# Performance work log

Hardware: AMD Instinct MI355X
Metric: run time of the kernel (lower is better)

Reference implementation:

```python
import jax, jax.numpy as jnp
import numpy as np

B, Q, K, QS, KS, H, DV = 16, 128, 512, 256, 256, 128, 256


def setup_inputs() -> dict:
    key = jax.random.key(0)
    ks = jax.random.split(key, 7)
    return {
        "queries": jax.random.normal(ks[0], (B, Q, QS), dtype=jnp.float32),
        "keys": jax.random.normal(ks[1], (B, K, KS), dtype=jnp.float32),
        "values": jax.random.normal(ks[2], (B, K, DV), dtype=jnp.float32),
        "valid_lens": jax.random.randint(ks[3], (B,), 1, K + 1),
        # Linear weights (no bias); stored as [in, hidden] so x @ W == nn.Linear
        "W_q": jax.random.normal(ks[4], (QS, H), dtype=jnp.float32) / np.float32(np.sqrt(QS)),
        "W_k": jax.random.normal(ks[5], (KS, H), dtype=jnp.float32) / np.float32(np.sqrt(KS)),
        "w_v": jax.random.normal(ks[6], (H,), dtype=jnp.float32) / np.float32(np.sqrt(H)),
    }


def reference(queries, keys, values, valid_lens, W_q, W_k, w_v):
    # Projections
    q = jnp.einsum('bqd,dh->bqh', queries, W_q)   # [B,Q,H]
    k = jnp.einsum('bkd,dh->bkh', keys, W_k)      # [B,K,H]
    # Additive (Bahdanau) score: tanh(q + k) . w_v  -> [B,Q,K]
    feats = jnp.tanh(q[:, :, None, :] + k[:, None, :, :])  # [B,Q,K,H] big intermediate
    scores = jnp.einsum('bqkh,h->bqk', feats, w_v)
    # masked softmax over keys: positions >= valid_len get -1e6 (as in torch ref)
    mask = jnp.arange(K)[None, None, :] < valid_lens[:, None, None]  # [B,1,K] bcast
    scores = jnp.where(mask, scores, jnp.float32(-1e6))
    attn = jax.nn.softmax(scores, axis=-1)        # [B,Q,K]
    # dropout p=0.0 -> identity
    return jnp.einsum('bqk,bkd->bqd', attn, values)  # [B,Q,DV]
```

## Files before the change

### kernel.cpp

```cpp
#include <hip/hip_runtime.h>
#include <hip/hip_bf16.h>

#define NB 16
#define NQ 128
#define NK 512
#define DIN 256
#define NH 128
#define NDV 256

#define CSC 2.8853900817779268f

__global__ __launch_bounds__(256) void proj_both_kernel(
    const float* __restrict__ Q, const float* __restrict__ K,
    const float* __restrict__ Wq, const float* __restrict__ Wk,
    float* __restrict__ QP, float* __restrict__ KPT)
{
    __shared__ float Xl[32 * DIN];
    const int tid = threadIdx.x;
    int blk = blockIdx.x;
    const float* X; const float* W;
    int b, r0, isq;
    if (blk < 64) { isq = 1; b = blk >> 2; r0 = (blk & 3) * 32;
                    X = Q + ((size_t)b * NQ + r0) * DIN; W = Wq; }
    else { blk -= 64; isq = 0; b = blk >> 4; r0 = (blk & 15) * 32;
           X = K + ((size_t)b * NK + r0) * DIN; W = Wk; }

    {
        const float4* Xg = (const float4*)X;
        float4* Xs = (float4*)Xl;
        #pragma unroll
        for (int i = 0; i < 8; ++i) Xs[tid + 256 * i] = Xg[tid + 256 * i];
    }
    __syncthreads();

    const int h4 = tid & 31;
    const int rg = tid >> 5;
    const float4* Wv = (const float4*)W;

    float4 acc[4];
    #pragma unroll
    for (int r = 0; r < 4; ++r) { acc[r].x = 0.f; acc[r].y = 0.f; acc[r].z = 0.f; acc[r].w = 0.f; }

    float4 w0 = Wv[0 * 32 + h4], w1 = Wv[1 * 32 + h4], w2 = Wv[2 * 32 + h4], w3 = Wv[3 * 32 + h4];
    float4 n0 = Wv[4 * 32 + h4], n1 = Wv[5 * 32 + h4], n2 = Wv[6 * 32 + h4], n3 = Wv[7 * 32 + h4];
    for (int d = 0; d < DIN; d += 4) {
        const int dp = (d + 8 < DIN) ? d + 8 : 0;
        float4 m0 = Wv[(dp + 0) * 32 + h4];
        float4 m1 = Wv[(dp + 1) * 32 + h4];
        float4 m2 = Wv[(dp + 2) * 32 + h4];
        float4 m3 = Wv[(dp + 3) * 32 + h4];
        #pragma unroll
        for (int r = 0; r < 4; ++r) {
            float4 x = *(const float4*)&Xl[(rg * 4 + r) * DIN + d];
            acc[r].x += x.x * w0.x + x.y * w1.x + x.z * w2.x + x.w * w3.x;
            acc[r].y += x.x * w0.y + x.y * w1.y + x.z * w2.y + x.w * w3.y;
            acc[r].z += x.x * w0.z + x.y * w1.z + x.z * w2.z + x.w * w3.z;
            acc[r].w += x.x * w0.w + x.y * w1.w + x.z * w2.w + x.w * w3.w;
        }
        w0 = n0; w1 = n1; w2 = n2; w3 = n3;
        n0 = m0; n1 = m1; n2 = m2; n3 = m3;
    }
    #pragma unroll
    for (int r = 0; r < 4; ++r) {
        acc[r].x *= CSC; acc[r].y *= CSC; acc[r].z *= CSC; acc[r].w *= CSC;
    }

    if (isq) {
        #pragma unroll
        for (int r = 0; r < 4; ++r)
            *(float4*)&QP[((size_t)b * NQ + r0 + rg * 4 + r) * NH + 4 * h4] = acc[r];
    } else {
        float* T = Xl;
        __syncthreads();
        #pragma unroll
        for (int r = 0; r < 4; ++r) {
            T[(4 * h4 + 0) * 36 + rg * 4 + r] = acc[r].x;
            T[(4 * h4 + 1) * 36 + rg * 4 + r] = acc[r].y;
            T[(4 * h4 + 2) * 36 + rg * 4 + r] = acc[r].z;
            T[(4 * h4 + 3) * 36 + rg * 4 + r] = acc[r].w;
        }
        __syncthreads();
        #pragma unroll
        for (int i = 0; i < 4; ++i) {
            const int idx = tid + 256 * i;
            const int h = idx >> 3, c8 = idx & 7;
            float4 v = *(const float4*)&T[h * 36 + c8 * 4];
            *(float4*)&KPT[((size_t)b * NH + h) * NK + r0 + c8 * 4] = v;
        }
    }
}

__global__ __launch_bounds__(512) void attn_fused_kernel(
    const float* __restrict__ QP, const float* __restrict__ KPT,
    const float* __restrict__ wv, const int* __restrict__ vlen,
    const float* __restrict__ V, float* __restrict__ OUT)
{
    __shared__ float qcl[4 * NH];
    __shared__ float wvl[NH];
    __shared__ float sc[4][NK];
    __shared__ float part[4][4][NDV];
    const int tid = threadIdx.x;
    const int b  = blockIdx.x & 15;
    const int q0 = (blockIdx.x >> 4) * 4;

    qcl[tid] = QP[((size_t)b * NQ + q0) * NH + tid];
    if (tid < NH) wvl[tid] = -2.0f * wv[tid];
    __syncthreads();

    int vl = vlen[b];
    vl = vl < 1 ? 1 : (vl > NK ? NK : vl);

    {
        const float* kb = KPT + (size_t)b * NH * NK + tid;
        float a0 = 0.f, a1 = 0.f, a2 = 0.f, a3 = 0.f;
        #pragma unroll 4
        for (int h = 0; h < NH; ++h) {
            float kv = kb[(size_t)h * NK];
            float wq = wvl[h];
            float e0 = __builtin_amdgcn_exp2f(qcl[0 * NH + h] + kv);
            float e1 = __builtin_amdgcn_exp2f(qcl[1 * NH + h] + kv);
            float e2 = __builtin_amdgcn_exp2f(qcl[2 * NH + h] + kv);
            float e3 = __builtin_amdgcn_exp2f(qcl[3 * NH + h] + kv);
            a0 += wq * __builtin_amdgcn_rcpf(e0 + 1.0f);
            a1 += wq * __builtin_amdgcn_rcpf(e1 + 1.0f);
            a2 += wq * __builtin_amdgcn_rcpf(e2 + 1.0f);
            a3 += wq * __builtin_amdgcn_rcpf(e3 + 1.0f);
        }
        const bool vld = (tid < vl);
        sc[0][tid] = vld ? a0 : -1e6f;
        sc[1][tid] = vld ? a1 : -1e6f;
        sc[2][tid] = vld ? a2 : -1e6f;
        sc[3][tid] = vld ? a3 : -1e6f;
    }
    __syncthreads();

    const int w = tid >> 6, lane = tid & 63;
    if (w < 4) {
        float vals[8];
        float m = -3.0e38f;
        #pragma unroll
        for (int i = 0; i < 8; ++i) { vals[i] = sc[w][lane + 64 * i]; m = fmaxf(m, vals[i]); }
        #pragma unroll
        for (int off = 32; off; off >>= 1) m = fmaxf(m, __shfl_xor(m, off, 64));
        float s = 0.f;
        #pragma unroll
        for (int i = 0; i < 8; ++i) {
            vals[i] = __builtin_amdgcn_exp2f((vals[i] - m) * 1.4426950408889634f);
            s += vals[i];
        }
        #pragma unroll
        for (int off = 32; off; off >>= 1) s += __shfl_xor(s, off, 64);
        const float invs = 1.0f / s;
        #pragma unroll
        for (int i = 0; i < 8; ++i) sc[w][lane + 64 * i] = vals[i] * invs;
    }
    __syncthreads();

    float4 o[4];
    #pragma unroll
    for (int r = 0; r < 4; ++r) { o[r].x = 0.f; o[r].y = 0.f; o[r].z = 0.f; o[r].w = 0.f; }
    {
        const float* vb = V + (size_t)b * NK * NDV + lane * 4;
        const int kb0 = w * 64;
        #pragma unroll 4
        for (int kk = 0; kk < 64; ++kk) {
            const int k = kb0 + kk;
            float4 v4 = *(const float4*)(vb + (size_t)k * NDV);
            float p0 = sc[0][k], p1 = sc[1][k], p2 = sc[2][k], p3 = sc[3][k];
            o[0].x += p0 * v4.x; o[0].y += p0 * v4.y; o[0].z += p0 * v4.z; o[0].w += p0 * v4.w;
            o[1].x += p1 * v4.x; o[1].y += p1 * v4.y; o[1].z += p1 * v4.z; o[1].w += p1 * v4.w;
            o[2].x += p2 * v4.x; o[2].y += p2 * v4.y; o[2].z += p2 * v4.z; o[2].w += p2 * v4.w;
            o[3].x += p3 * v4.x; o[3].y += p3 * v4.y; o[3].z += p3 * v4.z; o[3].w += p3 * v4.w;
        }
    }
    if (w >= 4) {
        #pragma unroll
        for (int r = 0; r < 4; ++r) *(float4*)&part[w - 4][r][lane * 4] = o[r];
    }
    __syncthreads();
    if (w < 4) {
        #pragma unroll
        for (int r = 0; r < 4; ++r) {
            float4 t = *(const float4*)&part[w][r][lane * 4];
            o[r].x += t.x; o[r].y += t.y; o[r].z += t.z; o[r].w += t.w;
            *(float4*)&part[w][r][lane * 4] = o[r];
        }
    }
    __syncthreads();
    if (tid < 256) {
        const int r = tid >> 6, d4 = tid & 63;
        float4 s = {0.f, 0.f, 0.f, 0.f};
        #pragma unroll
        for (int p = 0; p < 4; ++p) {
            float4 q = *(const float4*)&part[p][r][d4 * 4];
            s.x += q.x; s.y += q.y; s.z += q.z; s.w += q.w;
        }
        *(float4*)&OUT[((size_t)b * NQ + q0 + r) * NDV + d4 * 4] = s;
    }
}

extern "C" void kernel_launch(void* const* d_in, const int* in_sizes, int n_in,
                              void* d_out, int out_size, void* d_ws, size_t ws_size,
                              hipStream_t stream) {
    const float* queries = (const float*)d_in[0];
    const float* keys    = (const float*)d_in[1];
    const float* values  = (const float*)d_in[2];
    const int*   vlen    = (const int*)d_in[3];
    const float* Wq      = (const float*)d_in[4];
    const float* Wk      = (const float*)d_in[5];
    const float* wv      = (const float*)d_in[6];
    float* out           = (float*)d_out;

    float* qp  = (float*)d_ws;
    float* kpt = qp + (size_t)NB * NQ * NH;

    proj_both_kernel<<<64 + 256, 256, 0, stream>>>(queries, keys, Wq, Wk, qp, kpt);
    attn_fused_kernel<<<NB * 32, 512, 0, stream>>>(qp, kpt, wv, vlen, values, out);
}
```

Measured before the change: 131.6 us.

## Skip softmax max pass, defer normalization, prefetch keys, halve projection tiles

The attention kernel now exponentiates raw scores directly, with no max subtraction. This relies on the score being bounded, since it is a w_v-weighted sum of tanh values. Normalization by the row sum is deferred to the final output write, which removes one shared-memory pass and a reduction. The score loop gets explicit register prefetching of the next four key-projection rows. The projection kernel processes 16 rows per block instead of 32, doubling the grid for better CU occupancy. The trade-off is possible overflow if w_v has very large magnitude.

After: 135.1 us. 2.7% more time.

```diff
diff --git a/kernel.cpp b/kernel.cpp
--- a/kernel.cpp
+++ b/kernel.cpp
@@ -9,27 +9,28 @@
 #define NDV 256
 
 #define CSC 2.8853900817779268f
+#define L2E 1.4426950408889634f
 
 __global__ __launch_bounds__(256) void proj_both_kernel(
     const float* __restrict__ Q, const float* __restrict__ K,
     const float* __restrict__ Wq, const float* __restrict__ Wk,
     float* __restrict__ QP, float* __restrict__ KPT)
 {
-    __shared__ float Xl[32 * DIN];
+    __shared__ float Xl[16 * DIN];
     const int tid = threadIdx.x;
     int blk = blockIdx.x;
     const float* X; const float* W;
     int b, r0, isq;
-    if (blk < 64) { isq = 1; b = blk >> 2; r0 = (blk & 3) * 32;
-                    X = Q + ((size_t)b * NQ + r0) * DIN; W = Wq; }
-    else { blk -= 64; isq = 0; b = blk >> 4; r0 = (blk & 15) * 32;
+    if (blk < 128) { isq = 1; b = blk >> 3; r0 = (blk & 7) * 16;
+                     X = Q + ((size_t)b * NQ + r0) * DIN; W = Wq; }
+    else { blk -= 128; isq = 0; b = blk >> 5; r0 = (blk & 31) * 16;
            X = K + ((size_t)b * NK + r0) * DIN; W = Wk; }
 
     {
         const float4* Xg = (const float4*)X;
         float4* Xs = (float4*)Xl;
         #pragma unroll
-        for (int i = 0; i < 8; ++i) Xs[tid + 256 * i] = Xg[tid + 256 * i];
+        for (int i = 0; i < 4; ++i) Xs[tid + 256 * i] = Xg[tid + 256 * i];
     }
     __syncthreads();
 
@@ -37,9 +38,9 @@
     const int rg = tid >> 5;
     const float4* Wv = (const float4*)W;
 
-    float4 acc[4];
+    float4 acc[2];
     #pragma unroll
-    for (int r = 0; r < 4; ++r) { acc[r].x = 0.f; acc[r].y = 0.f; acc[r].z = 0.f; acc[r].w = 0.f; }
+    for (int r = 0; r < 2; ++r) { acc[r].x = 0.f; acc[r].y = 0.f; acc[r].z = 0.f; acc[r].w = 0.f; }
 
     float4 w0 = Wv[0 * 32 + h4], w1 = Wv[1 * 32 + h4], w2 = Wv[2 * 32 + h4], w3 = Wv[3 * 32 + h4];
     float4 n0 = Wv[4 * 32 + h4], n1 = Wv[5 * 32 + h4], n2 = Wv[6 * 32 + h4], n3 = Wv[7 * 32 + h4];
@@ -50,8 +51,8 @@
         float4 m2 = Wv[(dp + 2) * 32 + h4];
         float4 m3 = Wv[(dp + 3) * 32 + h4];
         #pragma unroll
-        for (int r = 0; r < 4; ++r) {
-            float4 x = *(const float4*)&Xl[(rg * 4 + r) * DIN + d];
+        for (int r = 0; r < 2; ++r) {
+            float4 x = *(const float4*)&Xl[(rg * 2 + r) * DIN + d];
             acc[r].x += x.x * w0.x + x.y * w1.x + x.z * w2.x + x.w * w3.x;
             acc[r].y += x.x * w0.y + x.y * w1.y + x.z * w2.y + x.w * w3.y;
             acc[r].z += x.x * w0.z + x.y * w1.z + x.z * w2.z + x.w * w3.z;
@@ -61,31 +62,31 @@
         n0 = m0; n1 = m1; n2 = m2; n3 = m3;
     }
     #pragma unroll
-    for (int r = 0; r < 4; ++r) {
+    for (int r = 0; r < 2; ++r) {
         acc[r].x *= CSC; acc[r].y *= CSC; acc[r].z *= CSC; acc[r].w *= CSC;
     }
 
     if (isq) {
         #pragma unroll
-        for (int r = 0; r < 4; ++r)
-            *(float4*)&QP[((size_t)b * NQ + r0 + rg * 4 + r) * NH + 4 * h4] = acc[r];
+        for (int r = 0; r < 2; ++r)
+            *(float4*)&QP[((size_t)b * NQ + r0 + rg * 2 + r) * NH + 4 * h4] = acc[r];
     } else {
         float* T = Xl;
         __syncthreads();
         #pragma unroll
-        for (int r = 0; r < 4; ++r) {
-            T[(4 * h4 + 0) * 36 + rg * 4 + r] = acc[r].x;
-            T[(4 * h4 + 1) * 36 + rg * 4 + r] = acc[r].y;
-            T[(4 * h4 + 2) * 36 + rg * 4 + r] = acc[r].z;
-            T[(4 * h4 + 3) * 36 + rg * 4 + r] = acc[r].w;
+        for (int r = 0; r < 2; ++r) {
+            T[(4 * h4 + 0) * 20 + rg * 2 + r] = acc[r].x;
+            T[(4 * h4 + 1) * 20 + rg * 2 + r] = acc[r].y;
+            T[(4 * h4 + 2) * 20 + rg * 2 + r] = acc[r].z;
+            T[(4 * h4 + 3) * 20 + rg * 2 + r] = acc[r].w;
         }
         __syncthreads();
         #pragma unroll
-        for (int i = 0; i < 4; ++i) {
+        for (int i = 0; i < 2; ++i) {
             const int idx = tid + 256 * i;
-            const int h = idx >> 3, c8 = idx & 7;
-            float4 v = *(const float4*)&T[h * 36 + c8 * 4];
-            *(float4*)&KPT[((size_t)b * NH + h) * NK + r0 + c8 * 4] = v;
+            const int h = idx >> 2, c4 = idx & 3;
+            float4 v = *(const float4*)&T[h * 20 + c4 * 4];
+            *(float4*)&KPT[((size_t)b * NH + h) * NK + r0 + c4 * 4] = v;
         }
     }
 }
@@ -99,6 +100,7 @@
     __shared__ float wvl[NH];
     __shared__ float sc[4][NK];
     __shared__ float part[4][4][NDV];
+    __shared__ float sinv[4];
     const int tid = threadIdx.x;
     const int b  = blockIdx.x & 15;
     const int q0 = (blockIdx.x >> 4) * 4;
@@ -113,46 +115,44 @@
     {
         const float* kb = KPT + (size_t)b * NH * NK + tid;
         float a0 = 0.f, a1 = 0.f, a2 = 0.f, a3 = 0.f;
-        #pragma unroll 4
-        for (int h = 0; h < NH; ++h) {
-            float kv = kb[(size_t)h * NK];
-            float wq = wvl[h];
-            float e0 = __builtin_amdgcn_exp2f(qcl[0 * NH + h] + kv);
-            float e1 = __builtin_amdgcn_exp2f(qcl[1 * NH + h] + kv);
-            float e2 = __builtin_amdgcn_exp2f(qcl[2 * NH + h] + kv);
-            float e3 = __builtin_amdgcn_exp2f(qcl[3 * NH + h] + kv);
-            a0 += wq * __builtin_amdgcn_rcpf(e0 + 1.0f);
-            a1 += wq * __builtin_amdgcn_rcpf(e1 + 1.0f);
-            a2 += wq * __builtin_amdgcn_rcpf(e2 + 1.0f);
-            a3 += wq * __builtin_amdgcn_rcpf(e3 + 1.0f);
+        float c0 = kb[0 * NK], c1 = kb[1 * NK], c2 = kb[2 * NK], c3 = kb[3 * NK];
+        for (int h = 0; h < NH; h += 4) {
+            const int hp = (h + 4 < NH) ? h + 4 : 0;
+            float p0 = kb[(size_t)(hp + 0) * NK];
+            float p1 = kb[(size_t)(hp + 1) * NK];
+            float p2 = kb[(size_t)(hp + 2) * NK];
+            float p3 = kb[(size_t)(hp + 3) * NK];
+            #pragma unroll
+            for (int j = 0; j < 4; ++j) {
+                const float kv = (j == 0) ? c0 : (j == 1) ? c1 : (j == 2) ? c2 : c3;
+                const float wq = wvl[h + j];
+                float e0 = __builtin_amdgcn_exp2f(qcl[0 * NH + h + j] + kv);
+                float e1 = __builtin_amdgcn_exp2f(qcl[1 * NH + h + j] + kv);
+                float e2 = __builtin_amdgcn_exp2f(qcl[2 * NH + h + j] + kv);
+                float e3 = __builtin_amdgcn_exp2f(qcl[3 * NH + h + j] + kv);
+                a0 += wq * __builtin_amdgcn_rcpf(e0 + 1.0f);
+                a1 += wq * __builtin_amdgcn_rcpf(e1 + 1.0f);
+                a2 += wq * __builtin_amdgcn_rcpf(e2 + 1.0f);
+                a3 += wq * __builtin_amdgcn_rcpf(e3 + 1.0f);
+            }
+            c0 = p0; c1 = p1; c2 = p2; c3 = p3;
         }
         const bool vld = (tid < vl);
-        sc[0][tid] = vld ? a0 : -1e6f;
-        sc[1][tid] = vld ? a1 : -1e6f;
-        sc[2][tid] = vld ? a2 : -1e6f;
-        sc[3][tid] = vld ? a3 : -1e6f;
+        sc[0][tid] = vld ? __builtin_amdgcn_exp2f(a0 * L2E) : 0.f;
+        sc[1][tid] = vld ? __builtin_amdgcn_exp2f(a1 * L2E) : 0.f;
+        sc[2][tid] = vld ? __builtin_amdgcn_exp2f(a2 * L2E) : 0.f;
+        sc[3][tid] = vld ? __builtin_amdgcn_exp2f(a3 * L2E) : 0.f;
     }
     __syncthreads();
 
     const int w = tid >> 6, lane = tid & 63;
     if (w < 4) {
-        float vals[8];
-        float m = -3.0e38f;
-        #pragma unroll
-        for (int i = 0; i < 8; ++i) { vals[i] = sc[w][lane + 64 * i]; m = fmaxf(m, vals[i]); }
-        #pragma unroll
-        for (int off = 32; off; off >>= 1) m = fmaxf(m, __shfl_xor(m, off, 64));
         float s = 0.f;
         #pragma unroll
-        for (int i = 0; i < 8; ++i) {
-            vals[i] = __builtin_amdgcn_exp2f((vals[i] - m) * 1.4426950408889634f);
-            s += vals[i];
-        }
+        for (int i = 0; i < 8; ++i) s += sc[w][lane + 64 * i];
         #pragma unroll
         for (int off = 32; off; off >>= 1) s += __shfl_xor(s, off, 64);
-        const float invs = 1.0f / s;
-        #pragma unroll
-        for (int i = 0; i < 8; ++i) sc[w][lane + 64 * i] = vals[i] * invs;
+        if (lane == 0) sinv[w] = __builtin_amdgcn_rcpf(s);
     }
     __syncthreads();
 
@@ -189,12 +189,14 @@
     __syncthreads();
     if (tid < 256) {
         const int r = tid >> 6, d4 = tid & 63;
+        const float iv = sinv[r];
         float4 s = {0.f, 0.f, 0.f, 0.f};
         #pragma unroll
         for (int p = 0; p < 4; ++p) {
             float4 q = *(const float4*)&part[p][r][d4 * 4];
             s.x += q.x; s.y += q.y; s.z += q.z; s.w += q.w;
         }
+        s.x *= iv; s.y *= iv; s.z *= iv; s.w *= iv;
         *(float4*)&OUT[((size_t)b * NQ + q0 + r) * NDV + d4 * 4] = s;
     }
 }
@@ -214,6 +216,6 @@
     float* qp  = (float*)d_ws;
     float* kpt = qp + (size_t)NB * NQ * NH;
 
-    proj_both_kernel<<<64 + 256, 256, 0, stream>>>(queries, keys, Wq, Wk, qp, kpt);
+    proj_both_kernel<<<128 + 512, 256, 0, stream>>>(queries, keys, Wq, Wk, qp, kpt);
     attn_fused_kernel<<<NB * 32, 512, 0, stream>>>(qp, kpt, wv, vlen, values, out);
 }
```
